# Optimization experiments

Measured on AMD Instinct MI355X. Metric: run time of the kernel, lower is better.

## Reference

```python
import jax, jax.numpy as jnp
import numpy as np
import math
from jax import lax

STRIDES = (8.0, 16.0, 32.0)
ANCHORS = (
    ((6.1, 8.1), (20.6, 12.6), (11.2, 23.7)),
    ((36.2, 26.8), (25.9, 57.2), (57.8, 47.9)),
    ((122.1, 78.3), (73.7, 143.8), (236.1, 213.1)),
)
NUM_CLASSES = 80
L = NUM_CLASSES + 5
NA = 3
SCORE_T = 0.1
NMS_T = 0.6
DETECTIONS = 100
TOPK = 1000          # static cap on post-threshold candidates per image
IMG = 640            # batched image H=W; also max_size used for class offsets


def setup_inputs() -> dict:
    key = jax.random.key(0)
    ks = jax.random.split(key, 8)
    N = 8
    chans = (128, 256, 512)
    hw = (80, 40, 20)
    inp = {}
    for i, (c, s) in enumerate(zip(chans, hw)):
        inp[f"f{i}"] = jax.random.normal(ks[i], (N, c, s, s), jnp.float32)
        inp[f"w{i}"] = jax.random.normal(ks[3 + i], (NA * L, c), jnp.float32) * 0.02
        b = np.zeros((NA, L), np.float32)
        b[:, 4] += math.log(8 / (416 / STRIDES[i]) ** 2)   # Predictor bias init
        b[:, 5:] += math.log(0.6 / (NUM_CLASSES - 0.99))
        inp[f"b{i}"] = jnp.asarray(b.reshape(-1))
    inp["scale_factors"] = jnp.ones((N,), jnp.float32)
    return inp


def _decode_level(f, w, b, stride, anchors):
    # f: [N,Cin,H,W]; w: [NA*L,Cin]; 1x1 conv == channel GEMM
    N, _, H, W = f.shape
    p = jnp.einsum('nchw,oc->nhwo', f, w) + b
    p = jax.nn.sigmoid(p.reshape(N, H, W, NA, L))
    gx, gy = jnp.meshgrid(jnp.arange(W, dtype=f.dtype), jnp.arange(H, dtype=f.dtype), indexing='xy')
    grid = jnp.stack((gx, gy), axis=-1)                       # [H,W,2] (x,y)
    xy = (2 * p[..., :2] - 0.5 + grid[None, :, :, None, :]) * stride
    wh = 4 * p[..., 2:4] ** 2 * anchors[None, None, None, :, :]
    box = jnp.concatenate((xy, wh), axis=-1).reshape(N, -1, 4)
    obj = p[..., 4].reshape(N, -1)
    cls = p[..., 5:].reshape(N, -1, NUM_CLASSES)
    return box, obj, cls


def _cxcywh2xyxy(b):
    cx, cy, w, h = b[..., 0], b[..., 1], b[..., 2], b[..., 3]
    return jnp.stack((cx - w / 2, cy - h / 2, cx + w / 2, cy + h / 2), axis=-1)


def _iou_one_many(b, boxes):
    lt = jnp.maximum(b[:2], boxes[:, :2])
    rb = jnp.minimum(b[2:], boxes[:, 2:])
    wh = jnp.clip(rb - lt, 0)
    inter = wh[:, 0] * wh[:, 1]
    area_b = (b[2] - b[0]) * (b[3] - b[1])
    areas = (boxes[:, 2] - boxes[:, 0]) * (boxes[:, 3] - boxes[:, 1])
    return inter / (area_b + areas - inter + 1e-7)


def _nms_fixed(boxes, scores):
    # greedy NMS, fixed DETECTIONS iterations; boxes already class-offset
    def step(valid, _):
        s = jnp.where(valid, scores, -jnp.inf)
        i = jnp.argmax(s)
        ok = s[i] > 0.0
        ious = _iou_one_many(boxes[i], boxes)
        nv = valid & (ious <= NMS_T)
        nv = nv.at[i].set(False)
        valid = jnp.where(ok, nv, valid)
        return valid, (jnp.where(ok, i, -1), ok)

    valid0 = scores > SCORE_T
    _, (idx, ok) = lax.scan(step, valid0, None, length=DETECTIONS)
    return idx, ok


def _per_image(boxes, obj, cls, sf):
    scores = obj[:, None] * cls                               # [A,C]
    mask = (obj[:, None] > SCORE_T) & (scores > SCORE_T)
    scores = jnp.where(mask, scores, -1.0)
    topv, topi = lax.top_k(scores.reshape(-1), TOPK)
    anchor = topi // NUM_CLASSES
    label = topi % NUM_CLASSES
    cb = boxes[anchor]
    cb = jnp.clip(cb, 0.0, float(IMG))                        # image_shapes = (IMG, IMG)
    off = cb + (label * IMG).astype(cb.dtype)[:, None]        # batched_nms class offset
    idx, ok = _nms_fixed(off, topv)
    gi = jnp.clip(idx, 0)
    okf = ok.astype(cb.dtype)
    out_box = cb[gi] / sf * okf[:, None]
    out_score = topv[gi] * okf
    out_label = label[gi].astype(cb.dtype) * okf
    return jnp.concatenate((out_box, out_score[:, None], out_label[:, None]), axis=1)  # [DET,6]


def reference(f0, f1, f2, w0, b0, w1, b1, w2, b2, scale_factors):
    feats = (f0, f1, f2)
    ws = (w0, w1, w2)
    bs = (b0, b1, b2)
    boxes, objs, clss = [], [], []
    for i in range(3):
        a = jnp.asarray(ANCHORS[i], dtype=f0.dtype)
        bx, ob, cl = _decode_level(feats[i], ws[i], bs[i], STRIDES[i], a)
        boxes.append(bx)
        objs.append(ob)
        clss.append(cl)
    boxes = _cxcywh2xyxy(jnp.concatenate(boxes, axis=1))      # [N, 25200, 4]
    obj = jnp.concatenate(objs, axis=1)                       # [N, 25200]
    cls = jnp.concatenate(clss, axis=1)                       # [N, 25200, 80]
    return jax.vmap(_per_image)(boxes, obj, cls, scale_factors)  # [N, DET, 6]
```

## Files before the change

### kernel.cpp

```cpp
#include <hip/hip_runtime.h>
#include <math.h>


#define NUM_CLASSES 80
#define IMG_F 640.0f

#define LOGITS_F 0
#define N_LOGITS 201600
#define WPACK_F  201600
#define N_WPACK  3584
#define CAND_F   (WPACK_F + N_WPACK)
#define CAP1     4096
#define CNT_F    (CAND_F + CAP1*2)
#define IMGBUF_F (CNT_F + 16)
#define CAP2     2048

__constant__ float d_anch[3][3][2] = {
  {{6.1f,8.1f},{20.6f,12.6f},{11.2f,23.7f}},
  {{36.2f,26.8f},{25.9f,57.2f},{57.8f,47.9f}},
  {{122.1f,78.3f},{73.7f,143.8f},{236.1f,213.1f}},
};
__constant__ float d_stridec[3] = {8.f,16.f,32.f};

__global__ __launch_bounds__(256) void k0_init(
    float* __restrict__ ws, float* __restrict__ out,
    const float* __restrict__ w0, const float* __restrict__ w1,
    const float* __restrict__ w2) {
  int i = blockIdx.x * 256 + threadIdx.x;
  if (i < N_LOGITS) ws[LOGITS_F + i] = 0.f;
  if (i < 4800)     out[i] = 0.f;
  if (i < 16)       ((int*)ws)[CNT_F + i] = 0;
  if (i < N_WPACK) {
    int a = i & 3, c4 = i >> 2;
    float v = 0.f;
    if (a < 3) {
      if (c4 < 128)       v = w0[(a*85+4)*128 + c4];
      else if (c4 < 384)  v = w1[(a*85+4)*256 + (c4-128)];
      else                v = w2[(a*85+4)*512 + (c4-384)];
    }
    ws[WPACK_F + i] = v;
  }
}

__global__ __launch_bounds__(256) void k1_obj(
    const float* __restrict__ f0, const float* __restrict__ f1,
    const float* __restrict__ f2, float* __restrict__ ws) {
  __shared__ float4 wl[128];
  int b = blockIdx.x, tid = threadIdx.x;
  int level, posblk, kc;
  if (b < 200)      { level = 0; posblk = b; kc = 0; }
  else if (b < 400) { int t = b - 200; level = 1; posblk = t % 50; kc = t / 50; }
  else              { int t = b - 400; level = 2; posblk = t % 13; kc = t / 13; }
  const int Cs[3]   = {128, 256, 512};
  const int HWs[3]  = {6400, 1600, 400};
  const int KBs[3]  = {1, 4, 8};
  const int AOFF[3] = {0, 19200, 24000};
  const int W4B[3]  = {0, 128, 384};
  int C = Cs[level], HW = HWs[level], KB = KBs[level];
  int chunk = C / KB;
  const float* f = (level == 0) ? f0 : (level == 1) ? f1 : f2;
  const float4* wp4 = (const float4*)(ws + WPACK_F);
  int c0 = kc * chunk;
  if (tid < chunk) wl[tid] = wp4[W4B[level] + c0 + tid];
  __syncthreads();
  int pos = posblk * 256 + tid;
  if (pos >= 8 * HW) return;
  int n = pos / HW, s = pos - n * HW;
  const float* fp = f + ((size_t)(n * C + c0)) * HW + s;
  float a0 = 0.f, a1 = 0.f, a2 = 0.f;
  #pragma unroll 8
  for (int c = 0; c < chunk; ++c) {
    float fv = fp[(size_t)c * HW];
    float4 w4 = wl[c];
    a0 = fmaf(fv, w4.x, a0);
    a1 = fmaf(fv, w4.y, a1);
    a2 = fmaf(fv, w4.z, a2);
  }
  float* lg = ws + LOGITS_F + n * 25200 + AOFF[level] + s * 3;
  if (KB == 1) { lg[0] = a0; lg[1] = a1; lg[2] = a2; }
  else { atomicAdd(lg, a0); atomicAdd(lg + 1, a1); atomicAdd(lg + 2, a2); }
}

__global__ __launch_bounds__(256) void k1b_thresh(
    float* __restrict__ ws, const float* __restrict__ b0,
    const float* __restrict__ b1, const float* __restrict__ b2) {
  int i = blockIdx.x * 256 + threadIdx.x;
  if (i >= N_LOGITS) return;
  int n = i / 25200, r = i - n * 25200;
  int level, roff;
  if (r < 19200)      { level = 0; roff = r; }
  else if (r < 24000) { level = 1; roff = r - 19200; }
  else                { level = 2; roff = r - 24000; }
  int s = roff / 3, a = roff - s * 3;
  const float* bb = (level == 0) ? b0 : (level == 1) ? b1 : b2;
  float logit = ws[LOGITS_F + i] + bb[a * 85 + 4];
  if (logit > -2.1972245773362196f) {
    float obj = 1.f / (1.f + expf(-logit));
    int idx = atomicAdd((int*)ws + CNT_F, 1);
    if (idx < CAP1) {
      int* cd = (int*)ws + CAND_F + idx * 2;
      cd[0] = (n << 24) | (level << 20) | (a << 16) | s;
      ((float*)cd)[1] = obj;
    }
  }
}

__global__ __launch_bounds__(256) void k2_score(
    const float* __restrict__ f0, const float* __restrict__ f1,
    const float* __restrict__ f2,
    const float* __restrict__ w0, const float* __restrict__ w1,
    const float* __restrict__ w2,
    const float* __restrict__ b0, const float* __restrict__ b1,
    const float* __restrict__ b2, float* __restrict__ ws) {
  __shared__ float fcol[4][512];
  __shared__ float pv[4][88];
  int wv = threadIdx.x >> 6, lane = threadIdx.x & 63;
  int cid = blockIdx.x * 4 + wv;
  int count = min(((int*)ws)[CNT_F], CAP1);
  bool active = cid < count;
  int level = 0, n = 0, a = 0, s = 0, C = 128, HW = 6400, Wd = 80;
  float obj = 0.f;
  const float *f = f0, *w = w0, *bb = b0;
  if (active) {
    int* cd = (int*)ws + CAND_F + cid * 2;
    int code = cd[0]; obj = ((float*)cd)[1];
    n = code >> 24; level = (code >> 20) & 15; a = (code >> 16) & 3; s = code & 0xFFFF;
    if (level == 1)      { C = 256; HW = 1600; Wd = 40; f = f1; w = w1; bb = b1; }
    else if (level == 2) { C = 512; HW = 400;  Wd = 20; f = f2; w = w2; bb = b2; }
    for (int c = lane; c < C; c += 64)
      fcol[wv][c] = f[((size_t)(n * C + c)) * HW + s];
  }
  __syncthreads();
  if (active) {
    for (int l = lane; l < 85; l += 64) {
      const float* wr = w + (size_t)(a * 85 + l) * C;
      float acc = bb[a * 85 + l];
      for (int c = 0; c < C; ++c) acc = fmaf(fcol[wv][c], wr[c], acc);
      pv[wv][l] = 1.f / (1.f + expf(-acc));
    }
  }
  __syncthreads();
  if (active) {
    float px = pv[wv][0], py = pv[wv][1], pw = pv[wv][2], ph = pv[wv][3];
    int gx = s % Wd, gy = s / Wd;
    float st = d_stridec[level];
    float cx = (2.f * px - 0.5f + (float)gx) * st;
    float cy = (2.f * py - 0.5f + (float)gy) * st;
    float bw = 4.f * pw * pw * d_anch[level][a][0];
    float bh = 4.f * ph * ph * d_anch[level][a][1];
    float x1 = fminf(fmaxf(cx - bw * 0.5f, 0.f), IMG_F);
    float y1 = fminf(fmaxf(cy - bh * 0.5f, 0.f), IMG_F);
    float x2 = fminf(fmaxf(cx + bw * 0.5f, 0.f), IMG_F);
    float y2 = fminf(fmaxf(cy + bh * 0.5f, 0.f), IMG_F);
    for (int l = lane; l < 85; l += 64) {
      if (l >= 5) {
        float sc = obj * pv[wv][l];
        if (sc > 0.1f) {
          int p = atomicAdd((int*)ws + CNT_F + 1 + n, 1);
          if (p < CAP2) {
            float* dst = ws + IMGBUF_F + ((size_t)(n * CAP2 + p)) * 6;
            dst[0] = x1; dst[1] = y1; dst[2] = x2; dst[3] = y2;
            dst[4] = sc; dst[5] = (float)(l - 5);
          }
        }
      }
    }
  }
}

__global__ __launch_bounds__(256) void k3_nms(
    const float* __restrict__ ws, float* __restrict__ out,
    const float* __restrict__ sfp) {
  __shared__ float bx1[CAP2], by1[CAP2], bx2[CAP2], by2[CAP2], bsc[CAP2], blb[CAP2];
  __shared__ int bval[CAP2];
  __shared__ float rs[256];
  __shared__ int ri[256];
  int n = blockIdx.x, tid = threadIdx.x;
  int cnt = min(((const int*)ws)[CNT_F + 1 + n], CAP2);
  for (int i = tid; i < cnt; i += 256) {
    const float* src = ws + IMGBUF_F + ((size_t)(n * CAP2 + i)) * 6;
    bx1[i] = src[0]; by1[i] = src[1]; bx2[i] = src[2]; by2[i] = src[3];
    bsc[i] = src[4]; blb[i] = src[5]; bval[i] = 1;
  }
  __syncthreads();
  float sf = sfp[n];
  for (int it = 0; it < 100; ++it) {
    float best = -1.f; int bi = -1;
    for (int i = tid; i < cnt; i += 256)
      if (bval[i] && bsc[i] > best) { best = bsc[i]; bi = i; }
    rs[tid] = best; ri[tid] = bi;
    __syncthreads();
    for (int off = 128; off > 0; off >>= 1) {
      if (tid < off && rs[tid + off] > rs[tid]) { rs[tid] = rs[tid + off]; ri[tid] = ri[tid + off]; }
      __syncthreads();
    }
    int wi = ri[0]; float wsc = rs[0];
    if (wi < 0) break;
    if (tid == 0) {
      float* o = out + (size_t)(n * 100 + it) * 6;
      o[0] = bx1[wi] / sf; o[1] = by1[wi] / sf;
      o[2] = bx2[wi] / sf; o[3] = by2[wi] / sf;
      o[4] = wsc;          o[5] = blb[wi];
    }
    float ofw = blb[wi] * IMG_F;
    float wx1 = bx1[wi] + ofw, wy1 = by1[wi] + ofw;
    float wx2 = bx2[wi] + ofw, wy2 = by2[wi] + ofw;
    float wa = (wx2 - wx1) * (wy2 - wy1);
    for (int i = tid; i < cnt; i += 256) {
      if (bval[i]) {
        float o2 = blb[i] * IMG_F;
        float x1 = bx1[i] + o2, y1 = by1[i] + o2, x2 = bx2[i] + o2, y2 = by2[i] + o2;
        float iw = fmaxf(fminf(wx2, x2) - fmaxf(wx1, x1), 0.f);
        float ih = fmaxf(fminf(wy2, y2) - fmaxf(wy1, y1), 0.f);
        float inter = iw * ih;
        float area = (x2 - x1) * (y2 - y1);
        float iou = inter / (wa + area - inter + 1e-7f);
        if (iou > 0.6f) bval[i] = 0;
      }
    }
    if (tid == 0) bval[wi] = 0;
    __syncthreads();
  }
}

extern "C" void kernel_launch(void* const* d_in, const int* in_sizes, int n_in,
                              void* d_out, int out_size, void* d_ws, size_t ws_size,
                              hipStream_t stream) {
  const float* f0 = (const float*)d_in[0];
  const float* w0 = (const float*)d_in[1];
  const float* b0 = (const float*)d_in[2];
  const float* f1 = (const float*)d_in[3];
  const float* w1 = (const float*)d_in[4];
  const float* b1 = (const float*)d_in[5];
  const float* f2 = (const float*)d_in[6];
  const float* w2 = (const float*)d_in[7];
  const float* b2 = (const float*)d_in[8];
  const float* sf = (const float*)d_in[9];
  float* out = (float*)d_out;
  float* ws  = (float*)d_ws;

  k0_init   <<<788, 256, 0, stream>>>(ws, out, w0, w1, w2);
  k1_obj    <<<504, 256, 0, stream>>>(f0, f1, f2, ws);
  k1b_thresh<<<788, 256, 0, stream>>>(ws, b0, b1, b2);
  k2_score  <<<1024, 256, 0, stream>>>(f0, f1, f2, w0, w1, w2, b0, b1, b2, ws);
  k3_nms    <<<8, 256, 0, stream>>>(ws, out, sf);
}
```

Baseline: 146.8 us.

## Fuse level-0 objectness threshold into GEMV and restructure candidate scoring per wave

Level-0 objectness logits are now thresholded directly inside k1_obj instead of being written to a logits buffer, which shrinks that buffer and the init/threshold passes to levels 1 and 2 only. k2_score is rewritten as a grid-stride loop over candidates with one wave per candidate. Each lane holds a slice of the feature column in registers and reduces every class dot product with wave shuffles, replacing the shared-memory staging where each lane looped over all channels. The grid shrinks from 1024 to 140 blocks. This removes global traffic and __syncthreads, but it serialises the 85 output channels, each with a shuffle reduction, inside each wave.

```diff
diff --git a/kernel.cpp b/kernel.cpp
--- a/kernel.cpp
+++ b/kernel.cpp
@@ -6,14 +6,16 @@
 #define IMG_F 640.0f
 
 #define LOGITS_F 0
-#define N_LOGITS 201600
-#define WPACK_F  201600
+#define N_LOGITS 48000
+#define WPACK_F  48000
 #define N_WPACK  3584
 #define CAND_F   (WPACK_F + N_WPACK)
 #define CAP1     4096
 #define CNT_F    (CAND_F + CAP1*2)
 #define IMGBUF_F (CNT_F + 16)
 #define CAP2     2048
+
+#define LOGIT_T (-2.1972245773362196f)
 
 __constant__ float d_anch[3][3][2] = {
   {{6.1f,8.1f},{20.6f,12.6f},{11.2f,23.7f}},
@@ -44,7 +46,8 @@
 
 __global__ __launch_bounds__(256) void k1_obj(
     const float* __restrict__ f0, const float* __restrict__ f1,
-    const float* __restrict__ f2, float* __restrict__ ws) {
+    const float* __restrict__ f2, const float* __restrict__ b0,
+    float* __restrict__ ws) {
   __shared__ float4 wl[128];
   int b = blockIdx.x, tid = threadIdx.x;
   int level, posblk, kc;
@@ -54,7 +57,6 @@
   const int Cs[3]   = {128, 256, 512};
   const int HWs[3]  = {6400, 1600, 400};
   const int KBs[3]  = {1, 4, 8};
-  const int AOFF[3] = {0, 19200, 24000};
   const int W4B[3]  = {0, 128, 384};
   int C = Cs[level], HW = HWs[level], KB = KBs[level];
   int chunk = C / KB;
@@ -67,34 +69,49 @@
   if (pos >= 8 * HW) return;
   int n = pos / HW, s = pos - n * HW;
   const float* fp = f + ((size_t)(n * C + c0)) * HW + s;
-  float a0 = 0.f, a1 = 0.f, a2 = 0.f;
-  #pragma unroll 8
+  float acc[3] = {0.f, 0.f, 0.f};
+  #pragma unroll 16
   for (int c = 0; c < chunk; ++c) {
     float fv = fp[(size_t)c * HW];
     float4 w4 = wl[c];
-    a0 = fmaf(fv, w4.x, a0);
-    a1 = fmaf(fv, w4.y, a1);
-    a2 = fmaf(fv, w4.z, a2);
-  }
-  float* lg = ws + LOGITS_F + n * 25200 + AOFF[level] + s * 3;
-  if (KB == 1) { lg[0] = a0; lg[1] = a1; lg[2] = a2; }
-  else { atomicAdd(lg, a0); atomicAdd(lg + 1, a1); atomicAdd(lg + 2, a2); }
+    acc[0] = fmaf(fv, w4.x, acc[0]);
+    acc[1] = fmaf(fv, w4.y, acc[1]);
+    acc[2] = fmaf(fv, w4.z, acc[2]);
+  }
+  if (level == 0) {
+    #pragma unroll
+    for (int a = 0; a < 3; ++a) {
+      float logit = acc[a] + b0[a * 85 + 4];
+      if (logit > LOGIT_T) {
+        float obj = 1.f / (1.f + expf(-logit));
+        int idx = atomicAdd((int*)ws + CNT_F, 1);
+        if (idx < CAP1) {
+          int* cd = (int*)ws + CAND_F + idx * 2;
+          cd[0] = (n << 24) | (0 << 20) | (a << 16) | s;
+          ((float*)cd)[1] = obj;
+        }
+      }
+    }
+  } else {
+    float* lg = ws + LOGITS_F + n * 6000 + ((level == 1) ? 0 : 4800) + s * 3;
+    atomicAdd(lg + 0, acc[0]);
+    atomicAdd(lg + 1, acc[1]);
+    atomicAdd(lg + 2, acc[2]);
+  }
 }
 
 __global__ __launch_bounds__(256) void k1b_thresh(
-    float* __restrict__ ws, const float* __restrict__ b0,
-    const float* __restrict__ b1, const float* __restrict__ b2) {
+    float* __restrict__ ws, const float* __restrict__ b1,
+    const float* __restrict__ b2) {
   int i = blockIdx.x * 256 + threadIdx.x;
   if (i >= N_LOGITS) return;
-  int n = i / 25200, r = i - n * 25200;
-  int level, roff;
-  if (r < 19200)      { level = 0; roff = r; }
-  else if (r < 24000) { level = 1; roff = r - 19200; }
-  else                { level = 2; roff = r - 24000; }
+  int n = i / 6000, r = i - n * 6000;
+  int level = (r < 4800) ? 1 : 2;
+  int roff = (r < 4800) ? r : r - 4800;
   int s = roff / 3, a = roff - s * 3;
-  const float* bb = (level == 0) ? b0 : (level == 1) ? b1 : b2;
+  const float* bb = (level == 1) ? b1 : b2;
   float logit = ws[LOGITS_F + i] + bb[a * 85 + 4];
-  if (logit > -2.1972245773362196f) {
+  if (logit > LOGIT_T) {
     float obj = 1.f / (1.f + expf(-logit));
     int idx = atomicAdd((int*)ws + CNT_F, 1);
     if (idx < CAP1) {
@@ -112,56 +129,55 @@
     const float* __restrict__ w2,
     const float* __restrict__ b0, const float* __restrict__ b1,
     const float* __restrict__ b2, float* __restrict__ ws) {
-  __shared__ float fcol[4][512];
-  __shared__ float pv[4][88];
   int wv = threadIdx.x >> 6, lane = threadIdx.x & 63;
-  int cid = blockIdx.x * 4 + wv;
   int count = min(((int*)ws)[CNT_F], CAP1);
-  bool active = cid < count;
-  int level = 0, n = 0, a = 0, s = 0, C = 128, HW = 6400, Wd = 80;
-  float obj = 0.f;
-  const float *f = f0, *w = w0, *bb = b0;
-  if (active) {
+  int nslots = gridDim.x * 4;
+  for (int cid = blockIdx.x * 4 + wv; cid < count; cid += nslots) {
     int* cd = (int*)ws + CAND_F + cid * 2;
-    int code = cd[0]; obj = ((float*)cd)[1];
-    n = code >> 24; level = (code >> 20) & 15; a = (code >> 16) & 3; s = code & 0xFFFF;
+    int code = cd[0]; float obj = ((float*)cd)[1];
+    int n = code >> 24, level = (code >> 20) & 15, a = (code >> 16) & 3, s = code & 0xFFFF;
+    int C = 128, HW = 6400, Wd = 80;
+    const float *f = f0, *w = w0, *bb = b0;
     if (level == 1)      { C = 256; HW = 1600; Wd = 40; f = f1; w = w1; bb = b1; }
     else if (level == 2) { C = 512; HW = 400;  Wd = 20; f = f2; w = w2; bb = b2; }
-    for (int c = lane; c < C; c += 64)
-      fcol[wv][c] = f[((size_t)(n * C + c)) * HW + s];
-  }
-  __syncthreads();
-  if (active) {
-    for (int l = lane; l < 85; l += 64) {
+    int J = C >> 6;
+    float fc[8];
+    for (int j = 0; j < J; ++j)
+      fc[j] = f[((size_t)(n * C + lane + 64 * j)) * HW + s];
+    float p03[4];
+    #pragma unroll
+    for (int l = 0; l < 4; ++l) {
       const float* wr = w + (size_t)(a * 85 + l) * C;
-      float acc = bb[a * 85 + l];
-      for (int c = 0; c < C; ++c) acc = fmaf(fcol[wv][c], wr[c], acc);
-      pv[wv][l] = 1.f / (1.f + expf(-acc));
-    }
-  }
-  __syncthreads();
-  if (active) {
-    float px = pv[wv][0], py = pv[wv][1], pw = pv[wv][2], ph = pv[wv][3];
+      float r = 0.f;
+      for (int j = 0; j < J; ++j) r = fmaf(fc[j], wr[lane + 64 * j], r);
+      #pragma unroll
+      for (int m = 32; m; m >>= 1) r += __shfl_xor(r, m, 64);
+      p03[l] = 1.f / (1.f + expf(-(r + bb[a * 85 + l])));
+    }
     int gx = s % Wd, gy = s / Wd;
     float st = d_stridec[level];
-    float cx = (2.f * px - 0.5f + (float)gx) * st;
-    float cy = (2.f * py - 0.5f + (float)gy) * st;
-    float bw = 4.f * pw * pw * d_anch[level][a][0];
-    float bh = 4.f * ph * ph * d_anch[level][a][1];
+    float cx = (2.f * p03[0] - 0.5f + (float)gx) * st;
+    float cy = (2.f * p03[1] - 0.5f + (float)gy) * st;
+    float bw = 4.f * p03[2] * p03[2] * d_anch[level][a][0];
+    float bh = 4.f * p03[3] * p03[3] * d_anch[level][a][1];
     float x1 = fminf(fmaxf(cx - bw * 0.5f, 0.f), IMG_F);
     float y1 = fminf(fmaxf(cy - bh * 0.5f, 0.f), IMG_F);
     float x2 = fminf(fmaxf(cx + bw * 0.5f, 0.f), IMG_F);
     float y2 = fminf(fmaxf(cy + bh * 0.5f, 0.f), IMG_F);
-    for (int l = lane; l < 85; l += 64) {
-      if (l >= 5) {
-        float sc = obj * pv[wv][l];
-        if (sc > 0.1f) {
-          int p = atomicAdd((int*)ws + CNT_F + 1 + n, 1);
-          if (p < CAP2) {
-            float* dst = ws + IMGBUF_F + ((size_t)(n * CAP2 + p)) * 6;
-            dst[0] = x1; dst[1] = y1; dst[2] = x2; dst[3] = y2;
-            dst[4] = sc; dst[5] = (float)(l - 5);
-          }
+    for (int l = 5; l < 85; ++l) {
+      const float* wr = w + (size_t)(a * 85 + l) * C;
+      float r = 0.f;
+      for (int j = 0; j < J; ++j) r = fmaf(fc[j], wr[lane + 64 * j], r);
+      #pragma unroll
+      for (int m = 32; m; m >>= 1) r += __shfl_xor(r, m, 64);
+      float cls = 1.f / (1.f + expf(-(r + bb[a * 85 + l])));
+      float sc = obj * cls;
+      if (sc > 0.1f && lane == 0) {
+        int p = atomicAdd((int*)ws + CNT_F + 1 + n, 1);
+        if (p < CAP2) {
+          float* dst = ws + IMGBUF_F + ((size_t)(n * CAP2 + p)) * 6;
+          dst[0] = x1; dst[1] = y1; dst[2] = x2; dst[3] = y2;
+          dst[4] = sc; dst[5] = (float)(l - 5);
         }
       }
     }
@@ -239,9 +255,9 @@
   float* out = (float*)d_out;
   float* ws  = (float*)d_ws;
 
-  k0_init   <<<788, 256, 0, stream>>>(ws, out, w0, w1, w2);
-  k1_obj    <<<504, 256, 0, stream>>>(f0, f1, f2, ws);
-  k1b_thresh<<<788, 256, 0, stream>>>(ws, b0, b1, b2);
-  k2_score  <<<1024, 256, 0, stream>>>(f0, f1, f2, w0, w1, w2, b0, b1, b2, ws);
+  k0_init   <<<188, 256, 0, stream>>>(ws, out, w0, w1, w2);
+  k1_obj    <<<504, 256, 0, stream>>>(f0, f1, f2, b0, ws);
+  k1b_thresh<<<188, 256, 0, stream>>>(ws, b1, b2);
+  k2_score  <<<140, 256, 0, stream>>>(f0, f1, f2, w0, w1, w2, b0, b1, b2, ws);
   k3_nms    <<<8, 256, 0, stream>>>(ws, out, sf);
 }
```

New measurement: 303.5 us. 107% more time.
